# Optimization experiments

Hardware: AMD Instinct MI355X
Metric: run time of the kernel (lower is better)

The kernel has to match this reference:

```python
import jax, jax.numpy as jnp
import numpy as np

N = 50000      # nodes
E = 800000     # edges (before self loops)
HID = 128      # hidden_dim
FEAT = 128     # feat_dim
NEG_SLOPE = 0.2
BN_EPS = 1e-5


def setup_inputs() -> dict:
    key = jax.random.key(0)
    ks = jax.random.split(key, 16)
    s = lambda d: 1.0 / np.sqrt(d).astype(np.float32)
    return {
        "x": jax.random.normal(ks[0], (N, HID), jnp.float32),
        "edge_index": jax.random.randint(ks[1], (2, E), 0, N, jnp.int32),
        # GATConv 1 (hidden -> hidden)
        "W1": jax.random.normal(ks[2], (HID, HID), jnp.float32) * s(HID),
        "att_src1": jax.random.normal(ks[3], (HID,), jnp.float32) * s(HID),
        "att_dst1": jax.random.normal(ks[4], (HID,), jnp.float32) * s(HID),
        "b1": jnp.zeros((HID,), jnp.float32),
        # BatchNorm1d(hidden) -- eval mode buffers/params
        "bn_gamma": jnp.ones((HID,), jnp.float32),
        "bn_beta": jnp.zeros((HID,), jnp.float32),
        "bn_mean": jax.random.normal(ks[5], (HID,), jnp.float32) * 0.1,
        "bn_var": jax.random.uniform(ks[6], (HID,), jnp.float32, 0.5, 1.5),
        # GATConv 2 (hidden -> feat)
        "W2": jax.random.normal(ks[7], (HID, FEAT), jnp.float32) * s(HID),
        "att_src2": jax.random.normal(ks[8], (FEAT,), jnp.float32) * s(FEAT),
        "att_dst2": jax.random.normal(ks[9], (FEAT,), jnp.float32) * s(FEAT),
        "b2": jnp.zeros((FEAT,), jnp.float32),
    }


def _gat_conv(x, W, att_src, att_dst, bias, src, dst, n_nodes):
    """PyG GATConv, heads=1: gather -> edge attn -> segment softmax -> scatter."""
    h = x @ W                                   # [N, d_out]
    a_s = h @ att_src                           # [N]
    a_d = h @ att_dst                           # [N]
    e = jax.nn.leaky_relu(a_s[src] + a_d[dst], NEG_SLOPE)  # [E']
    # numerically-stable softmax over incoming edges of each dst node
    e_max = jax.ops.segment_max(e, dst, num_segments=n_nodes)
    ex = jnp.exp(e - e_max[dst])
    denom = jax.ops.segment_sum(ex, dst, num_segments=n_nodes)
    alpha = ex / (denom[dst] + 1e-16)           # [E']
    out = jax.ops.segment_sum(alpha[:, None] * h[src], dst, num_segments=n_nodes)
    return out + bias


def reference(x, edge_index, W1, att_src1, att_dst1, b1,
              bn_gamma, bn_beta, bn_mean, bn_var,
              W2, att_src2, att_dst2, b2):
    n = x.shape[0]
    loops = jnp.arange(n, dtype=edge_index.dtype)
    src = jnp.concatenate([edge_index[0], loops])
    dst = jnp.concatenate([edge_index[1], loops])

    h = jax.nn.relu(_gat_conv(x, W1, att_src1, att_dst1, b1, src, dst, n))
    # BatchNorm1d in eval mode (running stats); dropout is identity in eval
    h = (h - bn_mean) * jax.lax.rsqrt(bn_var + BN_EPS) * bn_gamma + bn_beta
    out = jax.nn.relu(_gat_conv(h, W2, att_src2, att_dst2, b2, src, dst, n))
    return out
```

## Files before the change

### kernel.cpp

```cpp
#include <hip/hip_runtime.h>

typedef unsigned short u16;
typedef unsigned int   u32;

__device__ __forceinline__ float b2f(u16 h){ return __uint_as_float(((u32)h) << 16); }
__device__ __forceinline__ u16   f2b(float f){
  u32 u = __float_as_uint(f);
  u32 r = u + 0x7FFFu + ((u >> 16) & 1u);
  return (u16)(r >> 16);
}
__device__ __forceinline__ float lo16(u32 w){ return b2f((u16)(w & 0xFFFFu)); }
__device__ __forceinline__ float hi16(u32 w){ return b2f((u16)(w >> 16)); }

__global__ void r15_zero(int* p, int n){
  int t = blockIdx.x*blockDim.x + threadIdx.x;
  if (t < n) p[t] = 0;
}

__global__ void r15_hist(const int* ei, int E, int Ep, int* cnt){
  int t = blockIdx.x*blockDim.x + threadIdx.x;
  if (t >= Ep) return;
  int dst = (t < E) ? ei[E + t] : (t - E);
  atomicAdd(&cnt[dst], 1);
}

__global__ void r15_scan1(const int* in, int n, int* incl, int* bsums){
  __shared__ int tmp[256];
  int t = threadIdx.x; int g = blockIdx.x*256 + t;
  int v = (g < n) ? in[g] : 0;
  tmp[t] = v; __syncthreads();
  for (int off = 1; off < 256; off <<= 1){
    int u = (t >= off) ? tmp[t - off] : 0;
    __syncthreads();
    tmp[t] += u;
    __syncthreads();
  }
  if (g < n) incl[g] = tmp[t];
  if (t == 255) bsums[blockIdx.x] = tmp[255];
}

__global__ void r15_scan2(int* bsums, int nb){
  __shared__ int tmp[256];
  int t = threadIdx.x;
  int v = (t < nb) ? bsums[t] : 0;
  tmp[t] = v; __syncthreads();
  for (int off = 1; off < 256; off <<= 1){
    int u = (t >= off) ? tmp[t - off] : 0;
    __syncthreads();
    tmp[t] += u;
    __syncthreads();
  }
  if (t < nb) bsums[t] = tmp[t];
}

__global__ void r15_scan3(const int* incl, const int* cnt, const int* bsums,
                          int n, int Nnodes, int* offs, int* cursor){
  int t = threadIdx.x; int b = blockIdx.x; int g = b*256 + t;
  if (g >= n) return;
  int add = (b > 0) ? bsums[b-1] : 0;
  int ex = incl[g] - cnt[g] + add;
  offs[g] = ex;
  if (g < Nnodes) cursor[g] = ex;
}

__global__ __launch_bounds__(256)
void r15_gemm_fill(const float* __restrict__ X, const float* __restrict__ W,
                   const float* __restrict__ atts, const float* __restrict__ attd,
                   u16* __restrict__ HB, float* __restrict__ AS, float* __restrict__ AD,
                   int nrows, int gemmBlocks,
                   const int* __restrict__ ei, int E, int Ep,
                   int* cursor, int* csr_src){
  __shared__ float xs[64*128];
  int t = threadIdx.x;

  if ((int)blockIdx.x >= gemmBlocks){
    int g = ((int)blockIdx.x - gemmBlocks)*256 + t;
    if (g < Ep){
      int src, dst;
      if (g < E){ src = ei[g]; dst = ei[E + g]; } else { src = g - E; dst = g - E; }
      int pos = atomicAdd(&cursor[dst], 1);
      csr_src[pos] = src;
    }
    return;
  }

  int r0 = blockIdx.x * 64;
  #pragma unroll
  for (int it = 0; it < 8; ++it){
    int idx = it*256 + t;
    int row = idx >> 5;
    int c4  = (idx & 31) * 4;
    float4 v = {0.f,0.f,0.f,0.f};
    if (r0 + row < nrows) v = *(const float4*)(X + (size_t)(r0+row)*128 + c4);
    *(float4*)&xs[row*128 + c4] = v;
  }
  __syncthreads();

  int cgrp = t & 31, rgrp = t >> 5;
  int col0 = cgrp * 4;
  float acc[8][4];
  #pragma unroll
  for (int r = 0; r < 8; ++r){
    #pragma unroll
    for (int j = 0; j < 4; ++j) acc[r][j] = 0.f;
  }
  #pragma unroll 2
  for (int k = 0; k < 128; k += 4){
    float4 w0 = *(const float4*)(W + (size_t)(k+0)*128 + col0);
    float4 w1 = *(const float4*)(W + (size_t)(k+1)*128 + col0);
    float4 w2 = *(const float4*)(W + (size_t)(k+2)*128 + col0);
    float4 w3 = *(const float4*)(W + (size_t)(k+3)*128 + col0);
    float4 xr[8];
    #pragma unroll
    for (int r = 0; r < 8; ++r) xr[r] = *(const float4*)&xs[(rgrp*8 + r)*128 + k];
    #pragma unroll
    for (int r = 0; r < 8; ++r){
      acc[r][0] = fmaf(xr[r].x, w0.x, acc[r][0]);
      acc[r][1] = fmaf(xr[r].x, w0.y, acc[r][1]);
      acc[r][2] = fmaf(xr[r].x, w0.z, acc[r][2]);
      acc[r][3] = fmaf(xr[r].x, w0.w, acc[r][3]);
      acc[r][0] = fmaf(xr[r].y, w1.x, acc[r][0]);
      acc[r][1] = fmaf(xr[r].y, w1.y, acc[r][1]);
      acc[r][2] = fmaf(xr[r].y, w1.z, acc[r][2]);
      acc[r][3] = fmaf(xr[r].y, w1.w, acc[r][3]);
      acc[r][0] = fmaf(xr[r].z, w2.x, acc[r][0]);
      acc[r][1] = fmaf(xr[r].z, w2.y, acc[r][1]);
      acc[r][2] = fmaf(xr[r].z, w2.z, acc[r][2]);
      acc[r][3] = fmaf(xr[r].z, w2.w, acc[r][3]);
      acc[r][0] = fmaf(xr[r].w, w3.x, acc[r][0]);
      acc[r][1] = fmaf(xr[r].w, w3.y, acc[r][1]);
      acc[r][2] = fmaf(xr[r].w, w3.z, acc[r][2]);
      acc[r][3] = fmaf(xr[r].w, w3.w, acc[r][3]);
    }
  }
  float4 sv = *(const float4*)(atts + col0);
  float4 dv = *(const float4*)(attd + col0);
  #pragma unroll
  for (int r = 0; r < 8; ++r){
    int row = r0 + rgrp*8 + r;
    float ps = acc[r][0]*sv.x + acc[r][1]*sv.y + acc[r][2]*sv.z + acc[r][3]*sv.w;
    float pd = acc[r][0]*dv.x + acc[r][1]*dv.y + acc[r][2]*dv.z + acc[r][3]*dv.w;
    #pragma unroll
    for (int off = 16; off >= 1; off >>= 1){
      ps += __shfl_xor(ps, off);
      pd += __shfl_xor(pd, off);
    }
    if (row < nrows){
      uint2 pb;
      pb.x = (u32)f2b(acc[r][0]) | ((u32)f2b(acc[r][1]) << 16);
      pb.y = (u32)f2b(acc[r][2]) | ((u32)f2b(acc[r][3]) << 16);
      *(uint2*)&HB[(size_t)row*128 + col0] = pb;
      if (cgrp == 0){ AS[row] = ps; AD[row] = pd; }
    }
  }
}

__global__ __launch_bounds__(256)
void r15_gemm(const float* __restrict__ X, const float* __restrict__ W,
              const float* __restrict__ atts, const float* __restrict__ attd,
              u16* __restrict__ HB, float* __restrict__ AS, float* __restrict__ AD,
              int nrows){
  __shared__ float xs[64*128];
  int t = threadIdx.x;
  int r0 = blockIdx.x * 64;
  #pragma unroll
  for (int it = 0; it < 8; ++it){
    int idx = it*256 + t;
    int row = idx >> 5;
    int c4  = (idx & 31) * 4;
    float4 v = {0.f,0.f,0.f,0.f};
    if (r0 + row < nrows) v = *(const float4*)(X + (size_t)(r0+row)*128 + c4);
    *(float4*)&xs[row*128 + c4] = v;
  }
  __syncthreads();
  int cgrp = t & 31, rgrp = t >> 5;
  int col0 = cgrp * 4;
  float acc[8][4];
  #pragma unroll
  for (int r = 0; r < 8; ++r){
    #pragma unroll
    for (int j = 0; j < 4; ++j) acc[r][j] = 0.f;
  }
  #pragma unroll 2
  for (int k = 0; k < 128; k += 4){
    float4 w0 = *(const float4*)(W + (size_t)(k+0)*128 + col0);
    float4 w1 = *(const float4*)(W + (size_t)(k+1)*128 + col0);
    float4 w2 = *(const float4*)(W + (size_t)(k+2)*128 + col0);
    float4 w3 = *(const float4*)(W + (size_t)(k+3)*128 + col0);
    float4 xr[8];
    #pragma unroll
    for (int r = 0; r < 8; ++r) xr[r] = *(const float4*)&xs[(rgrp*8 + r)*128 + k];
    #pragma unroll
    for (int r = 0; r < 8; ++r){
      acc[r][0] = fmaf(xr[r].x, w0.x, acc[r][0]);
      acc[r][1] = fmaf(xr[r].x, w0.y, acc[r][1]);
      acc[r][2] = fmaf(xr[r].x, w0.z, acc[r][2]);
      acc[r][3] = fmaf(xr[r].x, w0.w, acc[r][3]);
      acc[r][0] = fmaf(xr[r].y, w1.x, acc[r][0]);
      acc[r][1] = fmaf(xr[r].y, w1.y, acc[r][1]);
      acc[r][2] = fmaf(xr[r].y, w1.z, acc[r][2]);
      acc[r][3] = fmaf(xr[r].y, w1.w, acc[r][3]);
      acc[r][0] = fmaf(xr[r].z, w2.x, acc[r][0]);
      acc[r][1] = fmaf(xr[r].z, w2.y, acc[r][1]);
      acc[r][2] = fmaf(xr[r].z, w2.z, acc[r][2]);
      acc[r][3] = fmaf(xr[r].z, w2.w, acc[r][3]);
      acc[r][0] = fmaf(xr[r].w, w3.x, acc[r][0]);
      acc[r][1] = fmaf(xr[r].w, w3.y, acc[r][1]);
      acc[r][2] = fmaf(xr[r].w, w3.z, acc[r][2]);
      acc[r][3] = fmaf(xr[r].w, w3.w, acc[r][3]);
    }
  }
  float4 sv = *(const float4*)(atts + col0);
  float4 dv = *(const float4*)(attd + col0);
  #pragma unroll
  for (int r = 0; r < 8; ++r){
    int row = r0 + rgrp*8 + r;
    float ps = acc[r][0]*sv.x + acc[r][1]*sv.y + acc[r][2]*sv.z + acc[r][3]*sv.w;
    float pd = acc[r][0]*dv.x + acc[r][1]*dv.y + acc[r][2]*dv.z + acc[r][3]*dv.w;
    #pragma unroll
    for (int off = 16; off >= 1; off >>= 1){
      ps += __shfl_xor(ps, off);
      pd += __shfl_xor(pd, off);
    }
    if (row < nrows){
      uint2 pb;
      pb.x = (u32)f2b(acc[r][0]) | ((u32)f2b(acc[r][1]) << 16);
      pb.y = (u32)f2b(acc[r][2]) | ((u32)f2b(acc[r][3]) << 16);
      *(uint2*)&HB[(size_t)row*128 + col0] = pb;
      if (cgrp == 0){ AS[row] = ps; AD[row] = pd; }
    }
  }
}

__global__ __launch_bounds__(256)
void r15_aggregate(const u16* __restrict__ HB, const float* __restrict__ AS,
                   const float* __restrict__ AD,
                   const int* __restrict__ offs, const int* __restrict__ csr,
                   const float* __restrict__ bias,
                   const float* __restrict__ gamma_, const float* __restrict__ beta_,
                   const float* __restrict__ mean_, const float* __restrict__ var_,
                   float* __restrict__ outp, int n, int doBN){
  int wid  = (blockIdx.x*256 + threadIdx.x) >> 6;
  int lane = threadIdx.x & 63;
  if (wid >= n) return;
  int beg = offs[wid], end = offs[wid+1];
  int deg = end - beg;
  float ad = AD[wid];
  int c2 = lane*2;
  float a0 = 0.f, a1 = 0.f;

  if (deg <= 64){
    int   my_s = 0;
    float my_e = -3.0e38f;
    int myk = beg + lane;
    bool act = (myk < end);
    if (act){
      my_s = csr[myk];
      float e = AS[my_s] + ad;
      my_e = (e > 0.f) ? e : 0.2f*e;
    }
    float m = my_e;
    #pragma unroll
    for (int off = 32; off >= 1; off >>= 1) m = fmaxf(m, __shfl_xor(m, off));
    float pz = act ? __expf(my_e - m) : 0.f;
    float den = pz;
    #pragma unroll
    for (int off = 32; off >= 1; off >>= 1) den += __shfl_xor(den, off);
    float my_al = pz / (den + 1e-16f);

    int j = 0;
    for (; j + 8 <= deg; j += 8){
      int   s0 = __shfl(my_s, j),   s1 = __shfl(my_s, j+1);
      int   s2 = __shfl(my_s, j+2), s3 = __shfl(my_s, j+3);
      int   s4 = __shfl(my_s, j+4), s5 = __shfl(my_s, j+5);
      int   s6 = __shfl(my_s, j+6), s7 = __shfl(my_s, j+7);
      float l0 = __shfl(my_al, j),   l1 = __shfl(my_al, j+1);
      float l2 = __shfl(my_al, j+2), l3 = __shfl(my_al, j+3);
      float l4 = __shfl(my_al, j+4), l5 = __shfl(my_al, j+5);
      float l6 = __shfl(my_al, j+6), l7 = __shfl(my_al, j+7);
      u32 h0 = *(const u32*)&HB[(size_t)s0*128 + c2];
      u32 h1 = *(const u32*)&HB[(size_t)s1*128 + c2];
      u32 h2 = *(const u32*)&HB[(size_t)s2*128 + c2];
      u32 h3 = *(const u32*)&HB[(size_t)s3*128 + c2];
      u32 h4 = *(const u32*)&HB[(size_t)s4*128 + c2];
      u32 h5 = *(const u32*)&HB[(size_t)s5*128 + c2];
      u32 h6 = *(const u32*)&HB[(size_t)s6*128 + c2];
      u32 h7 = *(const u32*)&HB[(size_t)s7*128 + c2];
      a0 = fmaf(l0, lo16(h0), a0); a1 = fmaf(l0, hi16(h0), a1);
      a0 = fmaf(l1, lo16(h1), a0); a1 = fmaf(l1, hi16(h1), a1);
      a0 = fmaf(l2, lo16(h2), a0); a1 = fmaf(l2, hi16(h2), a1);
      a0 = fmaf(l3, lo16(h3), a0); a1 = fmaf(l3, hi16(h3), a1);
      a0 = fmaf(l4, lo16(h4), a0); a1 = fmaf(l4, hi16(h4), a1);
      a0 = fmaf(l5, lo16(h5), a0); a1 = fmaf(l5, hi16(h5), a1);
      a0 = fmaf(l6, lo16(h6), a0); a1 = fmaf(l6, hi16(h6), a1);
      a0 = fmaf(l7, lo16(h7), a0); a1 = fmaf(l7, hi16(h7), a1);
    }
    for (; j + 4 <= deg; j += 4){
      int   s0 = __shfl(my_s, j),   s1 = __shfl(my_s, j+1);
      int   s2 = __shfl(my_s, j+2), s3 = __shfl(my_s, j+3);
      float l0 = __shfl(my_al, j),   l1 = __shfl(my_al, j+1);
      float l2 = __shfl(my_al, j+2), l3 = __shfl(my_al, j+3);
      u32 h0 = *(const u32*)&HB[(size_t)s0*128 + c2];
      u32 h1 = *(const u32*)&HB[(size_t)s1*128 + c2];
      u32 h2 = *(const u32*)&HB[(size_t)s2*128 + c2];
      u32 h3 = *(const u32*)&HB[(size_t)s3*128 + c2];
      a0 = fmaf(l0, lo16(h0), a0); a1 = fmaf(l0, hi16(h0), a1);
      a0 = fmaf(l1, lo16(h1), a0); a1 = fmaf(l1, hi16(h1), a1);
      a0 = fmaf(l2, lo16(h2), a0); a1 = fmaf(l2, hi16(h2), a1);
      a0 = fmaf(l3, lo16(h3), a0); a1 = fmaf(l3, hi16(h3), a1);
    }
    for (; j < deg; ++j){
      int   s = __shfl(my_s, j);
      float l = __shfl(my_al, j);
      u32 hv = *(const u32*)&HB[(size_t)s*128 + c2];
      a0 = fmaf(l, lo16(hv), a0); a1 = fmaf(l, hi16(hv), a1);
    }
  } else {
    float m = -3.0e38f;
    for (int k = beg + lane; k < end; k += 64){
      int s = csr[k];
      float e = AS[s] + ad; e = (e > 0.f) ? e : 0.2f*e;
      m = fmaxf(m, e);
    }
    #pragma unroll
    for (int off = 32; off >= 1; off >>= 1) m = fmaxf(m, __shfl_xor(m, off));
    float den = 0.f;
    for (int k = beg + lane; k < end; k += 64){
      int s = csr[k];
      float e = AS[s] + ad; e = (e > 0.f) ? e : 0.2f*e;
      den += __expf(e - m);
    }
    #pragma unroll
    for (int off = 32; off >= 1; off >>= 1) den += __shfl_xor(den, off);
    float inv = 1.0f / (den + 1e-16f);
    for (int k = beg; k < end; ++k){
      int s = csr[k];
      float e = AS[s] + ad; e = (e > 0.f) ? e : 0.2f*e;
      float al = __expf(e - m) * inv;
      u32 hv = *(const u32*)&HB[(size_t)s*128 + c2];
      a0 = fmaf(al, lo16(hv), a0); a1 = fmaf(al, hi16(hv), a1);
    }
  }

  float v0 = a0 + bias[c2];
  float v1 = a1 + bias[c2+1];
  v0 = fmaxf(v0, 0.f); v1 = fmaxf(v1, 0.f);
  if (doBN){
    float s0 = gamma_[c2]   * rsqrtf(var_[c2]   + 1e-5f);
    float s1 = gamma_[c2+1] * rsqrtf(var_[c2+1] + 1e-5f);
    v0 = (v0 - mean_[c2])*s0   + beta_[c2];
    v1 = (v1 - mean_[c2+1])*s1 + beta_[c2+1];
  }
  float2 o = {v0, v1};
  ((float2*)(outp + (size_t)wid*128))[lane] = o;
}

extern "C" void kernel_launch(void* const* d_in, const int* in_sizes, int n_in,
                              void* d_out, int out_size, void* d_ws, size_t ws_size,
                              hipStream_t stream){
  const float* x   = (const float*)d_in[0];
  const int*   ei  = (const int*)  d_in[1];
  const float* W1  = (const float*)d_in[2];
  const float* as1 = (const float*)d_in[3];
  const float* ad1 = (const float*)d_in[4];
  const float* b1  = (const float*)d_in[5];
  const float* bng = (const float*)d_in[6];
  const float* bnb = (const float*)d_in[7];
  const float* bnm = (const float*)d_in[8];
  const float* bnv = (const float*)d_in[9];
  const float* W2  = (const float*)d_in[10];
  const float* as2 = (const float*)d_in[11];
  const float* ad2 = (const float*)d_in[12];
  const float* b2  = (const float*)d_in[13];
  float* out = (float*)d_out;

  int N  = in_sizes[0] / 128;
  int E  = in_sizes[1] / 2;
  int Ep = E + N;
  if (N <= 0 || E <= 0) return;

  char* base = (char*)d_ws;
  size_t off = 0;
  auto alloc = [&](size_t bytes)->char*{
    off = (off + 255) & ~(size_t)255;
    char* q = base + off; off += bytes; return q;
  };
  float* AS     = (float*)alloc((size_t)N*4);
  float* AD     = (float*)alloc((size_t)N*4);
  int*   cnt    = (int*)  alloc((size_t)(N+1)*4);
  int*   offs   = (int*)  alloc((size_t)(N+1)*4);
  int*   cursor = (int*)  alloc((size_t)N*4);
  int*   bsums  = (int*)  alloc(1024);
  int*   csr    = (int*)  alloc((size_t)Ep*4);
  u16*   hb     = (u16*)  alloc((size_t)N*128*2);
  float* x2     = (float*)alloc((size_t)N*128*4);

  int n1 = N + 1;
  int zb = (n1 + 255)/256;
  int eb = (Ep + 255)/256;
  int sb = (n1 + 255)/256;
  int gb = (N + 63)/64;
  int wb = (N + 3)/4;

  r15_zero <<<zb, 256, 0, stream>>>(cnt, n1);
  r15_hist <<<eb, 256, 0, stream>>>(ei, E, Ep, cnt);
  r15_scan1<<<sb, 256, 0, stream>>>(cnt, n1, offs, bsums);
  r15_scan2<<<1, 256, 0, stream>>>(bsums, sb);
  r15_scan3<<<sb, 256, 0, stream>>>(offs, cnt, bsums, n1, N, offs, cursor);

  r15_gemm_fill<<<gb + eb, 256, 0, stream>>>(x, W1, as1, ad1, hb, AS, AD, N, gb,
                                             ei, E, Ep, cursor, csr);
  r15_aggregate<<<wb, 256, 0, stream>>>(hb, AS, AD, offs, csr, b1, bng, bnb, bnm, bnv,
                                        x2, N, 1);
  r15_gemm     <<<gb, 256, 0, stream>>>(x2, W2, as2, ad2, hb, AS, AD, N);
  r15_aggregate<<<wb, 256, 0, stream>>>(hb, AS, AD, offs, csr, b2, 0, 0, 0, 0,
                                        out, N, 0);
}
```

Before: 298.5 us.

## Use split-bf16 MFMA for node GEMMs with folded attention vectors

The scalar fp32 FMA GEMMs are replaced with a per-wave 16-row MFMA GEMM using bf16 hi/lo splitting (three MFMAs per tile) to keep near-fp32 accuracy. Weights are pre-split and transposed in a prep block fused into the histogram kernel. The attention logits are computed as x·(W·att) from precomputed vectors rather than reduced from h. The fill blocks are placed before the GEMM blocks in the fused launch. The aim is to cut GEMM compute time, at the cost of extra weight prep work and a small accuracy difference.

```diff
diff --git a/kernel.cpp b/kernel.cpp
--- a/kernel.cpp
+++ b/kernel.cpp
@@ -2,6 +2,8 @@
 
 typedef unsigned short u16;
 typedef unsigned int   u32;
+typedef __attribute__((ext_vector_type(8))) short bh8;
+typedef __attribute__((ext_vector_type(4))) float fx4;
 
 __device__ __forceinline__ float b2f(u16 h){ return __uint_as_float(((u32)h) << 16); }
 __device__ __forceinline__ u16   f2b(float f){
@@ -12,19 +14,61 @@
 __device__ __forceinline__ float lo16(u32 w){ return b2f((u16)(w & 0xFFFFu)); }
 __device__ __forceinline__ float hi16(u32 w){ return b2f((u16)(w >> 16)); }
 
-__global__ void r15_zero(int* p, int n){
+__global__ void r16_zero(int* p, int n){
   int t = blockIdx.x*blockDim.x + threadIdx.x;
   if (t < n) p[t] = 0;
 }
 
-__global__ void r15_hist(const int* ei, int E, int Ep, int* cnt){
-  int t = blockIdx.x*blockDim.x + threadIdx.x;
-  if (t >= Ep) return;
-  int dst = (t < E) ? ei[E + t] : (t - E);
+__global__ void r16_hist_prep(const int* __restrict__ ei, int E, int Ep, int* cnt,
+                              const float* __restrict__ W1, const float* __restrict__ as1,
+                              const float* __restrict__ ad1,
+                              const float* __restrict__ W2, const float* __restrict__ as2,
+                              const float* __restrict__ ad2,
+                              u16* __restrict__ w1H, u16* __restrict__ w1L,
+                              u16* __restrict__ w2H, u16* __restrict__ w2L,
+                              float* __restrict__ ws1, float* __restrict__ wd1,
+                              float* __restrict__ ws2, float* __restrict__ wd2){
+  int b = blockIdx.x;
+  int t = threadIdx.x;
+  if (b < 16){
+    const float* W = (b < 8) ? W1 : W2;
+    u16* HT = (b < 8) ? w1H : w2H;
+    u16* LT = (b < 8) ? w1L : w2L;
+    int n0 = (b & 7) * 16;
+    #pragma unroll
+    for (int it = 0; it < 8; ++it){
+      int idx = it*256 + t;
+      int n = n0 + (idx >> 7);
+      int k = idx & 127;
+      float w = W[(size_t)k*128 + n];
+      u16 h = f2b(w);
+      HT[(size_t)n*128 + k] = h;
+      LT[(size_t)n*128 + k] = f2b(w - b2f(h));
+    }
+    return;
+  }
+  if (b == 16){
+    int which = t >> 6;
+    const float* W   = (which < 2) ? W1 : W2;
+    const float* att = (which == 0) ? as1 : (which == 1) ? ad1 : (which == 2) ? as2 : ad2;
+    float* outv      = (which == 0) ? ws1 : (which == 1) ? wd1 : (which == 2) ? ws2 : wd2;
+    int k0 = (t & 63) * 2;
+    #pragma unroll
+    for (int kk = 0; kk < 2; ++kk){
+      int k = k0 + kk;
+      float s = 0.f;
+      for (int c = 0; c < 128; ++c) s = fmaf(W[(size_t)k*128 + c], att[c], s);
+      outv[k] = s;
+    }
+    return;
+  }
+  int g = (b - 17)*256 + t;
+  if (g >= Ep) return;
+  int dst = (g < E) ? ei[E + g] : (g - E);
   atomicAdd(&cnt[dst], 1);
 }
 
-__global__ void r15_scan1(const int* in, int n, int* incl, int* bsums){
+__global__ void r16_scan1(const int* in, int n, int* incl, int* bsums){
   __shared__ int tmp[256];
   int t = threadIdx.x; int g = blockIdx.x*256 + t;
   int v = (g < n) ? in[g] : 0;
@@ -39,7 +83,7 @@
   if (t == 255) bsums[blockIdx.x] = tmp[255];
 }
 
-__global__ void r15_scan2(int* bsums, int nb){
+__global__ void r16_scan2(int* bsums, int nb){
   __shared__ int tmp[256];
   int t = threadIdx.x;
   int v = (t < nb) ? bsums[t] : 0;
@@ -53,7 +97,7 @@
   if (t < nb) bsums[t] = tmp[t];
 }
 
-__global__ void r15_scan3(const int* incl, const int* cnt, const int* bsums,
+__global__ void r16_scan3(const int* incl, const int* cnt, const int* bsums,
                           int n, int Nnodes, int* offs, int* cursor){
   int t = threadIdx.x; int b = blockIdx.x; int g = b*256 + t;
   if (g >= n) return;
@@ -63,18 +107,83 @@
   if (g < Nnodes) cursor[g] = ex;
 }
 
+__device__ __forceinline__ void gemm16_wave(
+    const float* __restrict__ X, const u16* __restrict__ wH, const u16* __restrict__ wL,
+    const float* __restrict__ wsv, const float* __restrict__ wdv,
+    u16* __restrict__ HB, float* __restrict__ AS, float* __restrict__ AD,
+    int nrows, int w, int lane)
+{
+  int r0 = w * 16;
+  if (r0 >= nrows) return;
+  int rloc = lane & 15;
+  int q    = lane >> 4;
+  int myrow = r0 + rloc;
+  bool act = (myrow < nrows);
+  int rsafe = act ? myrow : (nrows - 1);
+
+  fx4 acc[8] = {};
+  float ds = 0.f, dd = 0.f;
+
+  const u16* wHrow = wH + (size_t)rloc * 128;
+  const u16* wLrow = wL + (size_t)rloc * 128;
+
+  #pragma unroll
+  for (int kk = 0; kk < 4; ++kk){
+    int kbase = kk*32 + q*8;
+    const float* xp = X + (size_t)rsafe*128 + kbase;
+    float4 xa = *(const float4*)xp;
+    float4 xb = *(const float4*)(xp + 4);
+    float xv[8] = {xa.x, xa.y, xa.z, xa.w, xb.x, xb.y, xb.z, xb.w};
+    if (!act){
+      #pragma unroll
+      for (int i = 0; i < 8; ++i) xv[i] = 0.f;
+    }
+    const float* sp = wsv + kbase;
+    const float* dp = wdv + kbase;
+    bh8 xh, xl;
+    #pragma unroll
+    for (int i = 0; i < 8; ++i){
+      ds = fmaf(xv[i], sp[i], ds);
+      dd = fmaf(xv[i], dp[i], dd);
+      u16 h = f2b(xv[i]);
+      xh[i] = (short)h;
+      xl[i] = (short)f2b(xv[i] - b2f(h));
+    }
+    #pragma unroll
+    for (int cf = 0; cf < 8; ++cf){
+      bh8 wh = *(const bh8*)(wHrow + (size_t)cf*2048 + kbase);
+      bh8 wl = *(const bh8*)(wLrow + (size_t)cf*2048 + kbase);
+      acc[cf] = __builtin_amdgcn_mfma_f32_16x16x32_bf16(wh, xh, acc[cf], 0, 0, 0);
+      acc[cf] = __builtin_amdgcn_mfma_f32_16x16x32_bf16(wl, xh, acc[cf], 0, 0, 0);
+      acc[cf] = __builtin_amdgcn_mfma_f32_16x16x32_bf16(wh, xl, acc[cf], 0, 0, 0);
+    }
+  }
+  ds += __shfl_xor(ds, 16); ds += __shfl_xor(ds, 32);
+  dd += __shfl_xor(dd, 16); dd += __shfl_xor(dd, 32);
+  if (act && q == 0){ AS[myrow] = ds; AD[myrow] = dd; }
+  if (act){
+    u16* hrow = HB + (size_t)myrow*128 + q*4;
+    #pragma unroll
+    for (int cf = 0; cf < 8; ++cf){
+      uint2 pb;
+      pb.x = (u32)f2b(acc[cf][0]) | ((u32)f2b(acc[cf][1]) << 16);
+      pb.y = (u32)f2b(acc[cf][2]) | ((u32)f2b(acc[cf][3]) << 16);
+      *(uint2*)(hrow + cf*16) = pb;
+    }
+  }
+}
+
 __global__ __launch_bounds__(256)
-void r15_gemm_fill(const float* __restrict__ X, const float* __restrict__ W,
-                   const float* __restrict__ atts, const float* __restrict__ attd,
+void r16_fill_gemm(const int* __restrict__ ei, int E, int Ep,
+                   int* cursor, int* __restrict__ csr_src,
+                   const float* __restrict__ X,
+                   const u16* __restrict__ wH, const u16* __restrict__ wL,
+                   const float* __restrict__ wsv, const float* __restrict__ wdv,
                    u16* __restrict__ HB, float* __restrict__ AS, float* __restrict__ AD,
-                   int nrows, int gemmBlocks,
-                   const int* __restrict__ ei, int E, int Ep,
-                   int* cursor, int* csr_src){
-  __shared__ float xs[64*128];
+                   int nrows, int fillBlocks){
   int t = threadIdx.x;
-
-  if ((int)blockIdx.x >= gemmBlocks){
-    int g = ((int)blockIdx.x - gemmBlocks)*256 + t;
+  if ((int)blockIdx.x < fillBlocks){
+    int g = (int)blockIdx.x*256 + t;
     if (g < Ep){
       int src, dst;
       if (g < E){ src = ei[g]; dst = ei[E + g]; } else { src = g - E; dst = g - E; }
@@ -83,157 +192,22 @@
     }
     return;
   }
-
-  int r0 = blockIdx.x * 64;
-  #pragma unroll
-  for (int it = 0; it < 8; ++it){
-    int idx = it*256 + t;
-    int row = idx >> 5;
-    int c4  = (idx & 31) * 4;
-    float4 v = {0.f,0.f,0.f,0.f};
-    if (r0 + row < nrows) v = *(const float4*)(X + (size_t)(r0+row)*128 + c4);
-    *(float4*)&xs[row*128 + c4] = v;
-  }
-  __syncthreads();
-
-  int cgrp = t & 31, rgrp = t >> 5;
-  int col0 = cgrp * 4;
-  float acc[8][4];
-  #pragma unroll
-  for (int r = 0; r < 8; ++r){
-    #pragma unroll
-    for (int j = 0; j < 4; ++j) acc[r][j] = 0.f;
-  }
-  #pragma unroll 2
-  for (int k = 0; k < 128; k += 4){
-    float4 w0 = *(const float4*)(W + (size_t)(k+0)*128 + col0);
-    float4 w1 = *(const float4*)(W + (size_t)(k+1)*128 + col0);
-    float4 w2 = *(const float4*)(W + (size_t)(k+2)*128 + col0);
-    float4 w3 = *(const float4*)(W + (size_t)(k+3)*128 + col0);
-    float4 xr[8];
-    #pragma unroll
-    for (int r = 0; r < 8; ++r) xr[r] = *(const float4*)&xs[(rgrp*8 + r)*128 + k];
-    #pragma unroll
-    for (int r = 0; r < 8; ++r){
-      acc[r][0] = fmaf(xr[r].x, w0.x, acc[r][0]);
-      acc[r][1] = fmaf(xr[r].x, w0.y, acc[r][1]);
-      acc[r][2] = fmaf(xr[r].x, w0.z, acc[r][2]);
-      acc[r][3] = fmaf(xr[r].x, w0.w, acc[r][3]);
-      acc[r][0] = fmaf(xr[r].y, w1.x, acc[r][0]);
-      acc[r][1] = fmaf(xr[r].y, w1.y, acc[r][1]);
-      acc[r][2] = fmaf(xr[r].y, w1.z, acc[r][2]);
-      acc[r][3] = fmaf(xr[r].y, w1.w, acc[r][3]);
-      acc[r][0] = fmaf(xr[r].z, w2.x, acc[r][0]);
-      acc[r][1] = fmaf(xr[r].z, w2.y, acc[r][1]);
-      acc[r][2] = fmaf(xr[r].z, w2.z, acc[r][2]);
-      acc[r][3] = fmaf(xr[r].z, w2.w, acc[r][3]);
-      acc[r][0] = fmaf(xr[r].w, w3.x, acc[r][0]);
-      acc[r][1] = fmaf(xr[r].w, w3.y, acc[r][1]);
-      acc[r][2] = fmaf(xr[r].w, w3.z, acc[r][2]);
-      acc[r][3] = fmaf(xr[r].w, w3.w, acc[r][3]);
-    }
-  }
-  float4 sv = *(const float4*)(atts + col0);
-  float4 dv = *(const float4*)(attd + col0);
-  #pragma unroll
-  for (int r = 0; r < 8; ++r){
-    int row = r0 + rgrp*8 + r;
-    float ps = acc[r][0]*sv.x + acc[r][1]*sv.y + acc[r][2]*sv.z + acc[r][3]*sv.w;
-    float pd = acc[r][0]*dv.x + acc[r][1]*dv.y + acc[r][2]*dv.z + acc[r][3]*dv.w;
-    #pragma unroll
-    for (int off = 16; off >= 1; off >>= 1){
-      ps += __shfl_xor(ps, off);
-      pd += __shfl_xor(pd, off);
-    }
-    if (row < nrows){
-      uint2 pb;
-      pb.x = (u32)f2b(acc[r][0]) | ((u32)f2b(acc[r][1]) << 16);
-      pb.y = (u32)f2b(acc[r][2]) | ((u32)f2b(acc[r][3]) << 16);
-      *(uint2*)&HB[(size_t)row*128 + col0] = pb;
-      if (cgrp == 0){ AS[row] = ps; AD[row] = pd; }
-    }
-  }
+  int w = ((int)blockIdx.x - fillBlocks)*4 + (t >> 6);
+  gemm16_wave(X, wH, wL, wsv, wdv, HB, AS, AD, nrows, w, t & 63);
 }
 
 __global__ __launch_bounds__(256)
-void r15_gemm(const float* __restrict__ X, const float* __restrict__ W,
-              const float* __restrict__ atts, const float* __restrict__ attd,
+void r16_gemm(const float* __restrict__ X,
+              const u16* __restrict__ wH, const u16* __restrict__ wL,
+              const float* __restrict__ wsv, const float* __restrict__ wdv,
               u16* __restrict__ HB, float* __restrict__ AS, float* __restrict__ AD,
               int nrows){
-  __shared__ float xs[64*128];
-  int t = threadIdx.x;
-  int r0 = blockIdx.x * 64;
-  #pragma unroll
-  for (int it = 0; it < 8; ++it){
-    int idx = it*256 + t;
-    int row = idx >> 5;
-    int c4  = (idx & 31) * 4;
-    float4 v = {0.f,0.f,0.f,0.f};
-    if (r0 + row < nrows) v = *(const float4*)(X + (size_t)(r0+row)*128 + c4);
-    *(float4*)&xs[row*128 + c4] = v;
-  }
-  __syncthreads();
-  int cgrp = t & 31, rgrp = t >> 5;
-  int col0 = cgrp * 4;
-  float acc[8][4];
-  #pragma unroll
-  for (int r = 0; r < 8; ++r){
-    #pragma unroll
-    for (int j = 0; j < 4; ++j) acc[r][j] = 0.f;
-  }
-  #pragma unroll 2
-  for (int k = 0; k < 128; k += 4){
-    float4 w0 = *(const float4*)(W + (size_t)(k+0)*128 + col0);
-    float4 w1 = *(const float4*)(W + (size_t)(k+1)*128 + col0);
-    float4 w2 = *(const float4*)(W + (size_t)(k+2)*128 + col0);
-    float4 w3 = *(const float4*)(W + (size_t)(k+3)*128 + col0);
-    float4 xr[8];
-    #pragma unroll
-    for (int r = 0; r < 8; ++r) xr[r] = *(const float4*)&xs[(rgrp*8 + r)*128 + k];
-    #pragma unroll
-    for (int r = 0; r < 8; ++r){
-      acc[r][0] = fmaf(xr[r].x, w0.x, acc[r][0]);
-      acc[r][1] = fmaf(xr[r].x, w0.y, acc[r][1]);
-      acc[r][2] = fmaf(xr[r].x, w0.z, acc[r][2]);
-      acc[r][3] = fmaf(xr[r].x, w0.w, acc[r][3]);
-      acc[r][0] = fmaf(xr[r].y, w1.x, acc[r][0]);
-      acc[r][1] = fmaf(xr[r].y, w1.y, acc[r][1]);
-      acc[r][2] = fmaf(xr[r].y, w1.z, acc[r][2]);
-      acc[r][3] = fmaf(xr[r].y, w1.w, acc[r][3]);
-      acc[r][0] = fmaf(xr[r].z, w2.x, acc[r][0]);
-      acc[r][1] = fmaf(xr[r].z, w2.y, acc[r][1]);
-      acc[r][2] = fmaf(xr[r].z, w2.z, acc[r][2]);
-      acc[r][3] = fmaf(xr[r].z, w2.w, acc[r][3]);
-      acc[r][0] = fmaf(xr[r].w, w3.x, acc[r][0]);
-      acc[r][1] = fmaf(xr[r].w, w3.y, acc[r][1]);
-      acc[r][2] = fmaf(xr[r].w, w3.z, acc[r][2]);
-      acc[r][3] = fmaf(xr[r].w, w3.w, acc[r][3]);
-    }
-  }
-  float4 sv = *(const float4*)(atts + col0);
-  float4 dv = *(const float4*)(attd + col0);
-  #pragma unroll
-  for (int r = 0; r < 8; ++r){
-    int row = r0 + rgrp*8 + r;
-    float ps = acc[r][0]*sv.x + acc[r][1]*sv.y + acc[r][2]*sv.z + acc[r][3]*sv.w;
-    float pd = acc[r][0]*dv.x + acc[r][1]*dv.y + acc[r][2]*dv.z + acc[r][3]*dv.w;
-    #pragma unroll
-    for (int off = 16; off >= 1; off >>= 1){
-      ps += __shfl_xor(ps, off);
-      pd += __shfl_xor(pd, off);
-    }
-    if (row < nrows){
-      uint2 pb;
-      pb.x = (u32)f2b(acc[r][0]) | ((u32)f2b(acc[r][1]) << 16);
-      pb.y = (u32)f2b(acc[r][2]) | ((u32)f2b(acc[r][3]) << 16);
-      *(uint2*)&HB[(size_t)row*128 + col0] = pb;
-      if (cgrp == 0){ AS[row] = ps; AD[row] = pd; }
-    }
-  }
+  int w = (int)blockIdx.x*4 + (threadIdx.x >> 6);
+  gemm16_wave(X, wH, wL, wsv, wdv, HB, AS, AD, nrows, w, threadIdx.x & 63);
 }
 
 __global__ __launch_bounds__(256)
-void r15_aggregate(const u16* __restrict__ HB, const float* __restrict__ AS,
+void r16_aggregate(const u16* __restrict__ HB, const float* __restrict__ AS,
                    const float* __restrict__ AD,
                    const int* __restrict__ offs, const int* __restrict__ csr,
                    const float* __restrict__ bias,
@@ -394,25 +368,38 @@
   int*   csr    = (int*)  alloc((size_t)Ep*4);
   u16*   hb     = (u16*)  alloc((size_t)N*128*2);
   float* x2     = (float*)alloc((size_t)N*128*4);
+  u16*   w1H    = (u16*)  alloc(128*128*2);
+  u16*   w1L    = (u16*)  alloc(128*128*2);
+  u16*   w2H    = (u16*)  alloc(128*128*2);
+  u16*   w2L    = (u16*)  alloc(128*128*2);
+  float* ws1    = (float*)alloc(128*4);
+  float* wd1    = (float*)alloc(128*4);
+  float* ws2    = (float*)alloc(128*4);
+  float* wd2    = (float*)alloc(128*4);
 
   int n1 = N + 1;
   int zb = (n1 + 255)/256;
   int eb = (Ep + 255)/256;
   int sb = (n1 + 255)/256;
-  int gb = (N + 63)/64;
+  int nW = (N + 15)/16;
+  int gwb = (nW + 3)/4;
   int wb = (N + 3)/4;
 
-  r15_zero <<<zb, 256, 0, stream>>>(cnt, n1);
-  r15_hist <<<eb, 256, 0, stream>>>(ei, E, Ep, cnt);
-  r15_scan1<<<sb, 256, 0, stream>>>(cnt, n1, offs, bsums);
-  r15_scan2<<<1, 256, 0, stream>>>(bsums, sb);
-  r15_scan3<<<sb, 256, 0, stream>>>(offs, cnt, bsums, n1, N, offs, cursor);
-
-  r15_gemm_fill<<<gb + eb, 256, 0, stream>>>(x, W1, as1, ad1, hb, AS, AD, N, gb,
-                                             ei, E, Ep, cursor, csr);
-  r15_aggregate<<<wb, 256, 0, stream>>>(hb, AS, AD, offs, csr, b1, bng, bnb, bnm, bnv,
+  r16_zero     <<<zb, 256, 0, stream>>>(cnt, n1);
+  r16_hist_prep<<<eb + 17, 256, 0, stream>>>(ei, E, Ep, cnt,
+                                             W1, as1, ad1, W2, as2, ad2,
+                                             w1H, w1L, w2H, w2L,
+                                             ws1, wd1, ws2, wd2);
+  r16_scan1<<<sb, 256, 0, stream>>>(cnt, n1, offs, bsums);
+  r16_scan2<<<1, 256, 0, stream>>>(bsums, sb);
+  r16_scan3<<<sb, 256, 0, stream>>>(offs, cnt, bsums, n1, N, offs, cursor);
+
+  r16_fill_gemm<<<eb + gwb, 256, 0, stream>>>(ei, E, Ep, cursor, csr,
+                                              x, w1H, w1L, ws1, wd1,
+                                              hb, AS, AD, N, eb);
+  r16_aggregate<<<wb, 256, 0, stream>>>(hb, AS, AD, offs, csr, b1, bng, bnb, bnm, bnv,
                                         x2, N, 1);
-  r15_gemm     <<<gb, 256, 0, stream>>>(x2, W2, as2, ad2, hb, AS, AD, N);
-  r15_aggregate<<<wb, 256, 0, stream>>>(hb, AS, AD, offs, csr, b2, 0, 0, 0, 0,
+  r16_gemm     <<<gwb, 256, 0, stream>>>(x2, w2H, w2L, ws2, wd2, hb, AS, AD, N);
+  r16_aggregate<<<wb, 256, 0, stream>>>(hb, AS, AD, offs, csr, b2, 0, 0, 0, 0,
                                         out, N, 0);
 }
```

After: 348.3 us. +16.7%, slower.
